# Kernel tuning notes

Hardware: AMD Instinct MI355X
Metric: run time of the kernel (lower is better)

## Reference

```python
import jax, jax.numpy as jnp
import numpy as np

NUM_HEADS = 8
NEG_INF = float(-2**32 + 1)  # matches torch padding value -2**32+1


def positional_encoding(B, T, d):
    # matches module: pe[:, :, 0::2] = sin(pos*div), pe[:, :, 1::2] = cos(pos*div)
    pos = jnp.arange(T, dtype=jnp.float32)[:, None]                      # (T, 1)
    div = jnp.exp(jnp.arange(0, d, 2, dtype=jnp.float32) * (-np.log(10000.0) / d))  # (d/2,)
    ang = pos * div                                                       # (T, d/2)
    pe = jnp.zeros((T, d), jnp.float32)
    pe = pe.at[:, 0::2].set(jnp.sin(ang)).at[:, 1::2].set(jnp.cos(ang))
    return jnp.broadcast_to(pe[None], (B, T, d))


def setup_inputs() -> dict:
    key = jax.random.key(0)
    ks = jax.random.split(key, 8)
    B, T, d, dff = 4, 2048, 128, 512
    s = 1.0 / np.sqrt(d)
    return {
        "x": jax.random.normal(ks[0], (B, T, d), jnp.float32),
        "W_Q": jax.random.normal(ks[1], (d, d), jnp.float32) * s,
        "W_K": jax.random.normal(ks[2], (d, d), jnp.float32) * s,
        "W_V": jax.random.normal(ks[3], (d, d), jnp.float32) * s,
        "W1": jax.random.normal(ks[4], (d, dff), jnp.float32) * s,
        "b1": jnp.zeros((dff,), jnp.float32),
        "W2": jax.random.normal(ks[5], (dff, d), jnp.float32) * (1.0 / np.sqrt(dff)),
        "b2": jnp.zeros((d,), jnp.float32),
    }


def reference(x, W_Q, W_K, W_V, W1, b1, W2, b2):
    B, T, d = x.shape
    H = NUM_HEADS
    e = d // H
    x = x + positional_encoding(B, T, d)           # residual later uses post-PE input
    Q = x @ W_Q
    K = x @ W_K
    V = x @ W_V
    # torch split(dim=2)+cat(dim=0) == (b t (h e)) -> (h b) t e; keep head axis separate
    Qh = Q.reshape(B, T, H, e).transpose(2, 0, 1, 3)   # (H, B, T, e)
    Kh = K.reshape(B, T, H, e).transpose(2, 0, 1, 3)
    Vh = V.reshape(B, T, H, e).transpose(2, 0, 1, 3)
    scores = jnp.einsum('hbqe,hbke->hbqk', Qh, Kh) / (T ** 0.5)  # scale by sqrt(time_step)
    mask = jnp.tril(jnp.ones((T, T), jnp.float32))
    scores = jnp.where(mask == 0, jnp.float32(NEG_INF), scores)
    # torch F.softmax(dim=1) on (H*B, T, T) -> softmax over QUERY axis (axis=2 here)
    attn = jax.nn.softmax(scores, axis=2)
    out = jnp.einsum('hbqk,hbke->hbqe', attn, Vh)      # (H, B, T, e)
    out = out.transpose(1, 2, 0, 3).reshape(B, T, d)   # cat heads back on feature dim
    ff = jnp.maximum(out @ W1 + b1, 0.0) @ W2 + b2
    return ff + x
```

## Files before the change

### kernel.cpp

```cpp
#include <hip/hip_runtime.h>
#include <math.h>
#include <stdint.h>

#define T_SEQ 2048
#define BATCH 4
#define DMODEL 128
#define DFF 512
#define NHEAD 8
#define EHEAD 16

#define QSCALE (0.022097086912079608f * 1.4426950408889634f)

typedef __attribute__((ext_vector_type(8))) short bf16x8;
typedef __attribute__((ext_vector_type(4))) short bf16x4;
typedef __attribute__((ext_vector_type(4))) float f32x4;

__device__ __forceinline__ short f2bf(float f) {
    uint32_t u = __float_as_uint(f);
    u = u + 0x7FFF + ((u >> 16) & 1);
    return (short)(u >> 16);
}
__device__ __forceinline__ short bftrunc(float f) {
    return (short)(__float_as_uint(f) >> 16);
}
__device__ __forceinline__ float bf2f(short s) {
    return __uint_as_float(((uint32_t)(unsigned short)s) << 16);
}
__device__ __forceinline__ float exp2_fast(float x) {
#if __has_builtin(__builtin_amdgcn_exp2f)
    return __builtin_amdgcn_exp2f(x);
#else
    float r; asm("v_exp_f32 %0, %1" : "=v"(r) : "v"(x)); return r;
#endif
}

#define MFMA16(A, B, C) __builtin_amdgcn_mfma_f32_16x16x32_bf16(A, B, C, 0, 0, 0)

__device__ __forceinline__ void gload16(const void* g, void* l) {
    __builtin_amdgcn_global_load_lds(
        (const __attribute__((address_space(1))) void*)g,
        (__attribute__((address_space(3))) void*)l, 16, 0, 0);
}

__device__ __forceinline__ int pair_rank(int id) {
    return (id < 256) ? id : 767 - id;
}

__global__ __launch_bounds__(256) void k_pre(const float* __restrict__ x,
                                             const float* __restrict__ WQ,
                                             const float* __restrict__ WK,
                                             const float* __restrict__ WV,
                                             const float* __restrict__ W1,
                                             const float* __restrict__ W2,
                                             float* __restrict__ xpe,
                                             short* __restrict__ xpe16,
                                             short* __restrict__ Wqkvt,
                                             short* __restrict__ W1t,
                                             short* __restrict__ W2t) {
    int bid = blockIdx.x;
    int tid = threadIdx.x;
    if (bid < 512) {
        int idx = bid * 256 + tid;
        int t = idx >> 6, fp = idx & 63;
        float dv = __expf(-(float)(2 * fp) * (9.210340371976184f / 128.0f));
        float ang = (float)t * dv;
        float sn = __sinf(ang), cs = __cosf(ang);
#pragma unroll
        for (int b = 0; b < 4; ++b) {
            size_t base = ((size_t)b * T_SEQ + t) * 128 + 2 * fp;
            float2 xv = *(const float2*)(x + base);
            float v0 = xv.x + sn, v1 = xv.y + cs;
            *(float2*)(xpe + base) = make_float2(v0, v1);
            uint32_t pk = (uint32_t)(unsigned short)f2bf(v0) |
                          ((uint32_t)(unsigned short)f2bf(v1) << 16);
            *(uint32_t*)(xpe16 + base) = pk;
        }
    } else if (bid < 704) {
        int m = (bid - 512) >> 6;
        int o = ((bid - 512) & 63) * 256 + tid;
        int n = o >> 7, k = o & 127;
        const float* W = (m == 0) ? WQ : (m == 1) ? WK : WV;
        Wqkvt[m * 16384 + o] = f2bf(W[k * 128 + n]);
    } else if (bid < 960) {
        int o = (bid - 704) * 256 + tid;
        int n = o >> 7, k = o & 127;
        W1t[o] = f2bf(W1[k * 512 + n]);
    } else {
        int o = (bid - 960) * 256 + tid;
        int n = o >> 9, k = o & 511;
        W2t[o] = f2bf(W2[k * 128 + n]);
    }
}

__global__ __launch_bounds__(256) void k_qkv(const short* __restrict__ xpe16,
                                             const short* __restrict__ Wqkvt,
                                             short* __restrict__ Qh,
                                             short* __restrict__ Kh,
                                             short* __restrict__ Vs) {
    int z = blockIdx.y;
    const short* Wt = Wqkvt + z * 16384;
    int wave = threadIdx.x >> 6, lane = threadIdx.x & 63;
    int g = lane >> 4, c = lane & 15;
    int row0 = blockIdx.x * 64 + wave * 16;

    bf16x8 wf[8][4];
#pragma unroll
    for (int nt = 0; nt < 8; ++nt)
#pragma unroll
        for (int kk = 0; kk < 4; ++kk)
            wf[nt][kk] = *(const bf16x8*)(Wt + (nt * 16 + c) * 128 + kk * 32 + 8 * g);

    bf16x8 af[4];
#pragma unroll
    for (int kk = 0; kk < 4; ++kk)
        af[kk] = *(const bf16x8*)(xpe16 + (size_t)(row0 + c) * 128 + kk * 32 + 8 * g);

    f32x4 acc[8];
#pragma unroll
    for (int nt = 0; nt < 8; ++nt) acc[nt] = (f32x4){0.f, 0.f, 0.f, 0.f};
#pragma unroll
    for (int kk = 0; kk < 4; ++kk)
#pragma unroll
        for (int nt = 0; nt < 8; ++nt)
            acc[nt] = MFMA16(af[kk], wf[nt][kk], acc[nt]);

    int b = row0 >> 11;
    int t0 = (row0 & (T_SEQ - 1)) + 4 * g;
    if (z < 2) {
        short* dst = (z == 0) ? Qh : Kh;
        float sc = (z == 0) ? QSCALE : 1.0f;
#pragma unroll
        for (int nt = 0; nt < 8; ++nt) {
            int hb = nt * 4 + b;
#pragma unroll
            for (int r = 0; r < 4; ++r)
                dst[(size_t)(hb * T_SEQ + t0 + r) * 16 + c] = f2bf(acc[nt][r] * sc);
        }
    } else {
#pragma unroll
        for (int nt = 0; nt < 8; ++nt) {
            int hb = nt * 4 + b;
            bf16x4 v;
#pragma unroll
            for (int r = 0; r < 4; ++r) v[r] = f2bf(acc[nt][r]);
            *(bf16x4*)(Vs + (size_t)(hb * 16 + c) * T_SEQ + t0) = v;
        }
    }
}

__global__ __launch_bounds__(512, 4) void k_csum(const short* __restrict__ Qh,
                                                 const short* __restrict__ Kh,
                                                 short* __restrict__ Vs) {
    __shared__ __align__(16) short Qt[2][4096];
    __shared__ float csLds[8][32];
    __shared__ float invl[128];
    const bf16x8 zz = {0, 0, 0, 0, 0, 0, 0, 0};
    const f32x4 z = {0.f, 0.f, 0.f, 0.f};

    int rank = pair_rank((int)blockIdx.x);
    int kc = rank >> 5, hb = rank & 31;
    int tid = threadIdx.x;
    int wave = tid >> 6, lane = tid & 63;
    int g = lane >> 4, c = lane & 15;
    int s = wave & 3, h = wave >> 2;
    int kw = kc * 128 + s * 32;
    const size_t hbT = (size_t)hb * T_SEQ;
    const short* Qg = Qh + hbT * 16;

    bf16x8 kfA = zz, kfB = zz;
    if (g < 2) {
        kfA = *(const bf16x8*)(Kh + (hbT + kw + c) * 16 + 8 * g);
        kfB = *(const bf16x8*)(Kh + (hbT + kw + 16 + c) * 16 + 8 * g);
    }

    int tstart = kc >> 1;
    gload16(Qg + (size_t)tstart * 4096 + tid * 8, &Qt[0][tid * 8]);
    __syncthreads();

    float csA = 0.f, csB = 0.f;
    for (int t = tstart; t < 8; ++t) {
        int buf = (t - tstart) & 1;
        if (t + 1 < 8)
            gload16(Qg + (size_t)(t + 1) * 4096 + tid * 8, &Qt[buf ^ 1][tid * 8]);
        const short* Qtb = &Qt[buf][0];
#pragma unroll
        for (int sj = 0; sj < 4; ++sj) {
            int ss = 4 * h + sj;
            int q32 = t * 256 + ss * 32;
            if (q32 + 31 < kw) continue;
            bf16x8 qfa = zz, qfb = zz;
            if (g < 2) {
                qfa = *(const bf16x8*)(Qtb + (ss * 32 + c) * 16 + g * 8);
                qfb = *(const bf16x8*)(Qtb + (ss * 32 + 16 + c) * 16 + g * 8);
            }
            f32x4 sA1 = MFMA16(qfa, kfA, z);
            f32x4 sB1 = MFMA16(qfa, kfB, z);
            f32x4 sA2 = MFMA16(qfb, kfA, z);
            f32x4 sB2 = MFMA16(qfb, kfB, z);
            if (q32 >= kw + 32) {
#pragma unroll
                for (int r = 0; r < 4; ++r) {
                    csA += exp2_fast(sA1[r]) + exp2_fast(sA2[r]);
                    csB += exp2_fast(sB1[r]) + exp2_fast(sB2[r]);
                }
            } else {
                int kA = kw + c, kB = kw + 16 + c;
#pragma unroll
                for (int r = 0; r < 4; ++r) {
                    int qa = q32 + 4 * g + r, qb = q32 + 16 + 4 * g + r;
                    csA += (qa >= kA) ? exp2_fast(sA1[r]) : 0.f;
                    csA += (qb >= kA) ? exp2_fast(sA2[r]) : 0.f;
                    csB += (qa >= kB) ? exp2_fast(sB1[r]) : 0.f;
                    csB += (qb >= kB) ? exp2_fast(sB2[r]) : 0.f;
                }
            }
        }
        __syncthreads();
    }

    csA += __shfl_xor(csA, 16);
    csA += __shfl_xor(csA, 32);
    csB += __shfl_xor(csB, 16);
    csB += __shfl_xor(csB, 32);
    if (lane < 32) csLds[wave][lane] = (lane < 16) ? csA : csB;
    __syncthreads();
    if (tid < 128) {
        int st = tid >> 5, col = tid & 31;
        invl[st * 32 + col] = 1.0f / (csLds[st][col] + csLds[st + 4][col]);
    }
    __syncthreads();
    if (tid < 256) {
        int e = tid >> 4, kcol = (tid & 15) * 8;
        size_t vo = (size_t)(hb * 16 + e) * T_SEQ + kc * 128 + kcol;
        bf16x8 v = *(bf16x8*)(Vs + vo);
        bf16x8 o;
#pragma unroll
        for (int j = 0; j < 8; ++j) o[j] = f2bf(bf2f(v[j]) * invl[kcol + j]);
        *(bf16x8*)(Vs + vo) = o;
    }
}

__global__ __launch_bounds__(512, 4) void k_attn(const short* __restrict__ Qh,
                                                 const short* __restrict__ Kh,
                                                 const short* __restrict__ Vs,
                                                 short* __restrict__ AObf) {
    __shared__ __align__(16) short Kt[2][4096];
    __shared__ __align__(16) short Vt[2][4096];
    const bf16x8 zz = {0, 0, 0, 0, 0, 0, 0, 0};
    const f32x4 z = {0.f, 0.f, 0.f, 0.f};

    int rank = pair_rank((int)blockIdx.x);
    int qn = 15 - (rank >> 5), hb = rank & 31;
    int h2 = hb >> 2, b = hb & 3;
    int tid = threadIdx.x;
    int wave = tid >> 6, lane = tid & 63;
    int g = lane >> 4, c = lane & 15;
    int s = wave & 3, h = wave >> 2;
    int q0w = qn * 128 + s * 32;
    const size_t hbT = (size_t)hb * T_SEQ;
    const short* Kg = Kh + hbT * 16;
    const short* Vg = Vs + (size_t)hb * 16 * T_SEQ;

    bf16x8 qf0 = zz, qf1 = zz;
    if (g < 2) {
        qf0 = *(const bf16x8*)(Qh + (hbT + q0w + c) * 16 + 8 * g);
        qf1 = *(const bf16x8*)(Qh + (hbT + q0w + 16 + c) * 16 + 8 * g);
    }

    int nT = (qn >> 1) + 1;

#define STAGE(bf, kt)                                                        \
    do {                                                                     \
        int k0s = (kt) * 256;                                                \
        gload16(Kg + (size_t)k0s * 16 + tid * 8, &Kt[bf][tid * 8]);          \
        int e0 = tid >> 5, jp = tid & 31, j0 = jp ^ (e0 & 7);                \
        gload16(Vg + (size_t)e0 * T_SEQ + k0s + j0 * 8, &Vt[bf][tid * 8]);   \
    } while (0)

    STAGE(0, 0);
    __syncthreads();

    f32x4 acc0 = z, acc1 = z;
    for (int t = 0; t < nT; ++t) {
        int buf = t & 1;
        if (t + 1 < nT) STAGE(buf ^ 1, t + 1);
        const short* Ktb = &Kt[buf][0];
        const short* Vtb = &Vt[buf][0];
#pragma unroll
        for (int sj = 0; sj < 4; ++sj) {
            int ss = 4 * h + sj;
            int k32 = t * 256 + ss * 32;
            if (k32 > q0w + 31) continue;
            bf16x8 kf0 = zz, kf1 = zz;
            if (g < 2) {
                kf0 = *(const bf16x8*)(Ktb + (ss * 32 + c) * 16 + g * 8);
                kf1 = *(const bf16x8*)(Ktb + (ss * 32 + 16 + c) * 16 + g * 8);
            }
            int ja = ss * 4 + (g >> 1);
            const short* vrow = Vtb + c * 256 + ((g & 1) << 2);
            bf16x4 v0 = *(const bf16x4*)(vrow + ((ja ^ (c & 7)) << 3));
            bf16x4 v1 = *(const bf16x4*)(vrow + (((ja + 2) ^ (c & 7)) << 3));
            f32x4 s0 = MFMA16(kf0, qf0, z);
            f32x4 s1 = MFMA16(kf1, qf0, z);
            f32x4 s2 = MFMA16(kf0, qf1, z);
            f32x4 s3 = MFMA16(kf1, qf1, z);
            bf16x8 aA, aB, vf;
            if (k32 + 31 <= q0w) {
#pragma unroll
                for (int r = 0; r < 4; ++r) {
                    aA[r] = bftrunc(exp2_fast(s0[r]));
                    aA[4 + r] = bftrunc(exp2_fast(s1[r]));
                    aB[r] = bftrunc(exp2_fast(s2[r]));
                    aB[4 + r] = bftrunc(exp2_fast(s3[r]));
                    vf[r] = v0[r];
                    vf[4 + r] = v1[r];
                }
            } else {
                int qa = q0w + c, qb = q0w + 16 + c;
                int ka = k32 + 4 * g, kb = k32 + 16 + 4 * g;
#pragma unroll
                for (int r = 0; r < 4; ++r) {
                    aA[r] = (ka + r <= qa) ? bftrunc(exp2_fast(s0[r])) : (short)0;
                    aA[4 + r] = (kb + r <= qa) ? bftrunc(exp2_fast(s1[r])) : (short)0;
                    aB[r] = (ka + r <= qb) ? bftrunc(exp2_fast(s2[r])) : (short)0;
                    aB[4 + r] = (kb + r <= qb) ? bftrunc(exp2_fast(s3[r])) : (short)0;
                    vf[r] = v0[r];
                    vf[4 + r] = v1[r];
                }
            }
            acc0 = MFMA16(aA, vf, acc0);
            acc1 = MFMA16(aB, vf, acc1);
        }
        __syncthreads();
    }
#undef STAGE

    float* Of = (float*)&Kt[0][0];
    if (h == 1) {
#pragma unroll
        for (int r = 0; r < 4; ++r) {
            Of[r * 256 + s * 64 + lane] = acc0[r];
            Of[(4 + r) * 256 + s * 64 + lane] = acc1[r];
        }
    }
    __syncthreads();
    if (h == 0) {
#pragma unroll
        for (int r = 0; r < 4; ++r) {
            acc0[r] += Of[r * 256 + s * 64 + lane];
            acc1[r] += Of[(4 + r) * 256 + s * 64 + lane];
        }
#pragma unroll
        for (int r = 0; r < 4; ++r) {
            AObf[(size_t)(b * T_SEQ + q0w + 4 * g + r) * DMODEL + h2 * EHEAD + c] = f2bf(acc0[r]);
            AObf[(size_t)(b * T_SEQ + q0w + 16 + 4 * g + r) * DMODEL + h2 * EHEAD + c] = f2bf(acc1[r]);
        }
    }
}

__global__ __launch_bounds__(256) void k_ff(const short* __restrict__ AObf,
                                            const short* __restrict__ W1t,
                                            const float* __restrict__ b1,
                                            const short* __restrict__ W2t,
                                            const float* __restrict__ b2,
                                            const float* __restrict__ xpe,
                                            float* __restrict__ out) {
    __shared__ __align__(16) short Fl[32][516];
    int w = threadIdx.x >> 6, lane = threadIdx.x & 63;
    int g = lane >> 4, c = lane & 15;
    int row0 = blockIdx.x * 32;

    {
        bf16x8 wf[8][4];
#pragma unroll
        for (int nt = 0; nt < 8; ++nt)
#pragma unroll
            for (int kk = 0; kk < 4; ++kk)
                wf[nt][kk] = *(const bf16x8*)(W1t + (w * 128 + nt * 16 + c) * 128 + kk * 32 + 8 * g);

#pragma unroll
        for (int ch = 0; ch < 2; ++ch) {
            int rbase = row0 + ch * 16;
            bf16x8 af[4];
#pragma unroll
            for (int kk = 0; kk < 4; ++kk)
                af[kk] = *(const bf16x8*)(AObf + (size_t)(rbase + c) * 128 + kk * 32 + 8 * g);

            f32x4 acc[8];
#pragma unroll
            for (int nt = 0; nt < 8; ++nt) acc[nt] = (f32x4){0.f, 0.f, 0.f, 0.f};
#pragma unroll
            for (int kk = 0; kk < 4; ++kk)
#pragma unroll
                for (int nt = 0; nt < 8; ++nt)
                    acc[nt] = MFMA16(af[kk], wf[nt][kk], acc[nt]);

#pragma unroll
            for (int nt = 0; nt < 8; ++nt) {
                int col = w * 128 + nt * 16 + c;
                float bb = b1[col];
#pragma unroll
                for (int r = 0; r < 4; ++r)
                    Fl[ch * 16 + 4 * g + r][col] = f2bf(fmaxf(acc[nt][r] + bb, 0.f));
            }
        }
    }
    __syncthreads();

    bf16x8 wf2[2][16];
#pragma unroll
    for (int nt = 0; nt < 2; ++nt)
#pragma unroll
        for (int kk = 0; kk < 16; ++kk)
            wf2[nt][kk] = *(const bf16x8*)(W2t + (w * 32 + nt * 16 + c) * 512 + kk * 32 + 8 * g);

#pragma unroll
    for (int ch = 0; ch < 2; ++ch) {
        int rbase = row0 + ch * 16;
        f32x4 acc2[2];
        acc2[0] = (f32x4){0.f, 0.f, 0.f, 0.f};
        acc2[1] = (f32x4){0.f, 0.f, 0.f, 0.f};
#pragma unroll
        for (int kk = 0; kk < 16; ++kk) {
            bf16x8 a = *(const bf16x8*)(&Fl[ch * 16 + c][kk * 32 + 8 * g]);
            acc2[0] = MFMA16(a, wf2[0][kk], acc2[0]);
            acc2[1] = MFMA16(a, wf2[1][kk], acc2[1]);
        }
#pragma unroll
        for (int nt = 0; nt < 2; ++nt) {
            int col = w * 32 + nt * 16 + c;
            float bb = b2[col];
#pragma unroll
            for (int r = 0; r < 4; ++r) {
                size_t o = (size_t)(rbase + 4 * g + r) * DMODEL + col;
                out[o] = acc2[nt][r] + bb + xpe[o];
            }
        }
    }
}

extern "C" void kernel_launch(void* const* d_in, const int* in_sizes, int n_in,
                              void* d_out, int out_size, void* d_ws, size_t ws_size,
                              hipStream_t stream) {
    const float* x  = (const float*)d_in[0];
    const float* WQ = (const float*)d_in[1];
    const float* WK = (const float*)d_in[2];
    const float* WV = (const float*)d_in[3];
    const float* W1 = (const float*)d_in[4];
    const float* b1 = (const float*)d_in[5];
    const float* W2 = (const float*)d_in[6];
    const float* b2 = (const float*)d_in[7];
    float* out = (float*)d_out;

    const size_t NTD = (size_t)BATCH * T_SEQ * DMODEL;
    float* xpe   = (float*)d_ws;
    short* xpe16 = (short*)(xpe + NTD);
    short* Qh    = xpe16 + NTD;
    short* Kh    = Qh + NTD;
    short* Vs    = Kh + NTD;
    short* AObf  = Vs + NTD;
    short* Wqkvt = AObf + NTD;
    short* W1t   = Wqkvt + 3 * 16384;
    short* W2t   = W1t + 65536;

    k_pre<<<dim3(1216), dim3(256), 0, stream>>>(x, WQ, WK, WV, W1, W2,
                                                xpe, xpe16, Wqkvt, W1t, W2t);

    k_qkv<<<dim3(128, 3), dim3(256), 0, stream>>>(xpe16, Wqkvt, Qh, Kh, Vs);

    k_csum<<<dim3(512), dim3(512), 0, stream>>>(Qh, Kh, Vs);

    k_attn<<<dim3(512), dim3(512), 0, stream>>>(Qh, Kh, Vs, AObf);

    k_ff<<<dim3(256), dim3(256), 0, stream>>>(AObf, W1t, b1, W2t, b2, xpe, out);
}
```

Measured before the change: 64.40 us.

## Fuse positional-encoding and weight conversion into QKV projection kernel

```diff
diff --git a/kernel.cpp b/kernel.cpp
--- a/kernel.cpp
+++ b/kernel.cpp
@@ -46,74 +46,92 @@
     return (id < 256) ? id : 767 - id;
 }
 
-__global__ __launch_bounds__(256) void k_pre(const float* __restrict__ x,
+#define WP 136
+__global__ __launch_bounds__(256) void k_qkv(const float* __restrict__ x,
                                              const float* __restrict__ WQ,
                                              const float* __restrict__ WK,
                                              const float* __restrict__ WV,
                                              const float* __restrict__ W1,
                                              const float* __restrict__ W2,
                                              float* __restrict__ xpe,
-                                             short* __restrict__ xpe16,
-                                             short* __restrict__ Wqkvt,
+                                             short* __restrict__ Qh,
+                                             short* __restrict__ Kh,
+                                             short* __restrict__ Vs,
                                              short* __restrict__ W1t,
                                              short* __restrict__ W2t) {
-    int bid = blockIdx.x;
+    __shared__ __align__(16) short Wlds[128 * WP];
+    int z = blockIdx.y;
     int tid = threadIdx.x;
-    if (bid < 512) {
-        int idx = bid * 256 + tid;
-        int t = idx >> 6, fp = idx & 63;
-        float dv = __expf(-(float)(2 * fp) * (9.210340371976184f / 128.0f));
-        float ang = (float)t * dv;
-        float sn = __sinf(ang), cs = __cosf(ang);
-#pragma unroll
-        for (int b = 0; b < 4; ++b) {
-            size_t base = ((size_t)b * T_SEQ + t) * 128 + 2 * fp;
-            float2 xv = *(const float2*)(x + base);
-            float v0 = xv.x + sn, v1 = xv.y + cs;
-            *(float2*)(xpe + base) = make_float2(v0, v1);
-            uint32_t pk = (uint32_t)(unsigned short)f2bf(v0) |
-                          ((uint32_t)(unsigned short)f2bf(v1) << 16);
-            *(uint32_t*)(xpe16 + base) = pk;
-        }
-    } else if (bid < 704) {
-        int m = (bid - 512) >> 6;
-        int o = ((bid - 512) & 63) * 256 + tid;
-        int n = o >> 7, k = o & 127;
-        const float* W = (m == 0) ? WQ : (m == 1) ? WK : WV;
-        Wqkvt[m * 16384 + o] = f2bf(W[k * 128 + n]);
-    } else if (bid < 960) {
-        int o = (bid - 704) * 256 + tid;
-        int n = o >> 7, k = o & 127;
-        W1t[o] = f2bf(W1[k * 512 + n]);
-    } else {
-        int o = (bid - 960) * 256 + tid;
-        int n = o >> 9, k = o & 511;
-        W2t[o] = f2bf(W2[k * 128 + n]);
-    }
-}
-
-__global__ __launch_bounds__(256) void k_qkv(const short* __restrict__ xpe16,
-                                             const short* __restrict__ Wqkvt,
-                                             short* __restrict__ Qh,
-                                             short* __restrict__ Kh,
-                                             short* __restrict__ Vs) {
-    int z = blockIdx.y;
-    const short* Wt = Wqkvt + z * 16384;
-    int wave = threadIdx.x >> 6, lane = threadIdx.x & 63;
+
+    if (z == 3) {
+        int base = (int)blockIdx.x * 256 + tid;
+#pragma unroll
+        for (int i = 0; i < 2; ++i) {
+            int o = base + i * 32768;
+            int n = o >> 7, k = o & 127;
+            W1t[o] = f2bf(W1[k * 512 + n]);
+        }
+#pragma unroll
+        for (int i = 0; i < 2; ++i) {
+            int o = base + i * 32768;
+            int n = o >> 9, k = o & 511;
+            W2t[o] = f2bf(W2[k * 128 + n]);
+        }
+        return;
+    }
+
+    int wave = tid >> 6, lane = tid & 63;
     int g = lane >> 4, c = lane & 15;
     int row0 = blockIdx.x * 64 + wave * 16;
+    int row = row0 + c;
+    int tloc = row & (T_SEQ - 1);
+
+    {
+        const float* Wsrc = (z == 0) ? WQ : (z == 1) ? WK : WV;
+        int k = tid & 127, n0 = (tid >> 7) * 64;
+        const float* src = Wsrc + k * 128 + n0;
+#pragma unroll
+        for (int j = 0; j < 64; j += 4) {
+            float4 wv = *(const float4*)(src + j);
+            Wlds[(n0 + j + 0) * WP + k] = f2bf(wv.x);
+            Wlds[(n0 + j + 1) * WP + k] = f2bf(wv.y);
+            Wlds[(n0 + j + 2) * WP + k] = f2bf(wv.z);
+            Wlds[(n0 + j + 3) * WP + k] = f2bf(wv.w);
+        }
+    }
+
+    bf16x8 af[4];
+#pragma unroll
+    for (int kk = 0; kk < 4; ++kk) {
+        int d0 = kk * 32 + 8 * g;
+        const float* xb = x + (size_t)row * 128 + d0;
+        float4 xa = *(const float4*)(xb);
+        float4 xc = *(const float4*)(xb + 4);
+        float vv[8] = {xa.x, xa.y, xa.z, xa.w, xc.x, xc.y, xc.z, xc.w};
+#pragma unroll
+        for (int p = 0; p < 4; ++p) {
+            int d = d0 + 2 * p;
+            float dv = __expf(-(float)d * (9.210340371976184f / 128.0f));
+            float ang = (float)tloc * dv;
+            vv[2 * p] += __sinf(ang);
+            vv[2 * p + 1] += __cosf(ang);
+        }
+        if (z == 0) {
+            float* xo = xpe + (size_t)row * 128 + d0;
+            *(float4*)(xo) = make_float4(vv[0], vv[1], vv[2], vv[3]);
+            *(float4*)(xo + 4) = make_float4(vv[4], vv[5], vv[6], vv[7]);
+        }
+#pragma unroll
+        for (int j = 0; j < 8; ++j) af[kk][j] = f2bf(vv[j]);
+    }
+    __syncthreads();
 
     bf16x8 wf[8][4];
 #pragma unroll
     for (int nt = 0; nt < 8; ++nt)
 #pragma unroll
         for (int kk = 0; kk < 4; ++kk)
-            wf[nt][kk] = *(const bf16x8*)(Wt + (nt * 16 + c) * 128 + kk * 32 + 8 * g);
-
-    bf16x8 af[4];
-#pragma unroll
-    for (int kk = 0; kk < 4; ++kk)
-        af[kk] = *(const bf16x8*)(xpe16 + (size_t)(row0 + c) * 128 + kk * 32 + 8 * g);
+            wf[nt][kk] = *(const bf16x8*)(&Wlds[(nt * 16 + c) * WP + kk * 32 + 8 * g]);
 
     f32x4 acc[8];
 #pragma unroll
@@ -147,6 +165,7 @@
         }
     }
 }
+#undef WP
 
 __global__ __launch_bounds__(512, 4) void k_csum(const short* __restrict__ Qh,
                                                  const short* __restrict__ Kh,
@@ -454,19 +473,15 @@
 
     const size_t NTD = (size_t)BATCH * T_SEQ * DMODEL;
     float* xpe   = (float*)d_ws;
-    short* xpe16 = (short*)(xpe + NTD);
-    short* Qh    = xpe16 + NTD;
+    short* Qh    = (short*)(xpe + NTD);
     short* Kh    = Qh + NTD;
     short* Vs    = Kh + NTD;
     short* AObf  = Vs + NTD;
-    short* Wqkvt = AObf + NTD;
-    short* W1t   = Wqkvt + 3 * 16384;
+    short* W1t   = AObf + NTD;
     short* W2t   = W1t + 65536;
 
-    k_pre<<<dim3(1216), dim3(256), 0, stream>>>(x, WQ, WK, WV, W1, W2,
-                                                xpe, xpe16, Wqkvt, W1t, W2t);
-
-    k_qkv<<<dim3(128, 3), dim3(256), 0, stream>>>(xpe16, Wqkvt, Qh, Kh, Vs);
+    k_qkv<<<dim3(128, 4), dim3(256), 0, stream>>>(x, WQ, WK, WV, W1, W2,
+                                                  xpe, Qh, Kh, Vs, W1t, W2t);
 
     k_csum<<<dim3(512), dim3(512), 0, stream>>>(Qh, Kh, Vs);
 
```

Result: faster. 59.53 us (-7.6%).
